# Kernel optimization log

Measured on AMD Instinct MI355X. Metric: run time of the kernel, lower is better.

## Reference

```python
import jax, jax.numpy as jnp
import numpy as np

B = 256          # graphs per batch
NN = 400         # ROI nodes per graph (N*(N-1)/2 = 79800 = input_dim)
HID = [32, 64, 128]
KS = [200, 100, 50]   # nodes kept after each TopKPooling (ratio 0.5 each)
EPS = 1e-5


def setup_inputs() -> dict:
    key = jax.random.key(0)
    ks = jax.random.split(key, 20)
    # flattened strict upper triangle of a nonnegative FC matrix per sample
    data = jax.random.uniform(ks[0], (B, NN * (NN - 1) // 2), dtype=jnp.float32)
    inp = {"data": data}
    dims = [1] + HID
    for l in range(3):
        fan_in = dims[l]
        inp[f"W{l+1}"] = jax.random.normal(ks[1 + 5 * l], (dims[l], dims[l + 1]), jnp.float32) / np.sqrt(fan_in)
        inp[f"b{l+1}"] = jnp.zeros((dims[l + 1],), jnp.float32)
        inp[f"g{l+1}"] = jnp.ones((dims[l + 1],), jnp.float32)      # BN gamma
        inp[f"be{l+1}"] = jnp.zeros((dims[l + 1],), jnp.float32)    # BN beta
        inp[f"p{l+1}"] = jax.random.normal(ks[4 + 5 * l], (dims[l + 1],), jnp.float32) * 0.1  # TopK score vector
    return inp


def _gcn_conv(A, X, W, b):
    # GCNConv with edge weights: add self loops (weight 1), symmetric D^-1/2 A D^-1/2
    n = A.shape[1]
    Al = A + jnp.eye(n, dtype=A.dtype)[None]          # (B, n, n)
    deg = Al.sum(axis=-1)                             # (B, n)
    dis = jnp.where(deg > 0, jax.lax.rsqrt(deg), 0.0)
    An = dis[:, :, None] * Al * dis[:, None, :]
    return jnp.einsum('bij,bjf->bif', An, X @ W) + b


def _block(A, X, W, b, g, be, p, k):
    # GCNConv -> ReLU -> BatchNorm(train stats) -> (dropout=identity) -> TopKPooling
    h = jax.nn.relu(_gcn_conv(A, X, W, b))
    mu = h.mean(axis=(0, 1))
    var = h.var(axis=(0, 1))
    h = (h - mu) * jax.lax.rsqrt(var + EPS) * g + be
    # TopKPooling: score = x . p / ||p||, keep top k per graph, gate by tanh(score)
    score = h @ p / jnp.linalg.norm(p)                # (B, n)
    vals, idx = jax.lax.top_k(score, k)               # (B, k)
    Xn = jnp.take_along_axis(h, idx[:, :, None], axis=1) * jnp.tanh(vals)[:, :, None]
    bi = jnp.arange(A.shape[0])[:, None, None]
    An = A[bi, idx[:, :, None], idx[:, None, :]]      # filter_adj: edges among kept nodes
    return An, Xn


def reference(data, W1, b1, g1, be1, p1, W2, b2, g2, be2, p2, W3, b3, g3, be3, p3):
    Bn = data.shape[0]
    iu0, iu1 = np.triu_indices(NN, 1)
    A = jnp.zeros((Bn, NN, NN), data.dtype).at[:, iu0, iu1].set(data)
    A = A + jnp.swapaxes(A, 1, 2)                     # symmetric FC adjacency, zero diag
    X = jnp.ones((Bn, NN, 1), data.dtype)             # initial node feature dim = 1
    A, X = _block(A, X, W1, b1, g1, be1, p1, KS[0])
    A, X = _block(A, X, W2, b2, g2, be2, p2, KS[1])
    A, X = _block(A, X, W3, b3, g3, be3, p3, KS[2])
    return X.max(axis=1)                              # global_max_pool -> (B, 128)
```

## Files before the change

kernel.cpp:

```cpp
#include <hip/hip_runtime.h>
#include <math.h>

#define BB   256
#define NN0  400
#define NE   79800
#define EPSF 1e-5f

__device__ __forceinline__ int tri_e(int a, int c) {
  return a*(NN0-1) - ((a*(a-1))>>1) + (c - a - 1);
}

__device__ __forceinline__ size_t PRI(int b, int ti, int tj, int r) {
  return (((size_t)b*7 + ti)*7 + tj)*64 + r;
}

__device__ __forceinline__ float wave_sum(float v) {
  #pragma unroll
  for (int o = 32; o > 0; o >>= 1) v += __shfl_xor(v, o, 64);
  return v;
}

__device__ __forceinline__ void bitonic_desc(float* sc, int* si, int P) {
  const int tid = threadIdx.x;
  const int nt = blockDim.x;
  for (int k = 2; k <= P; k <<= 1) {
    for (int j = k >> 1; j > 0; j >>= 1) {
      __syncthreads();
      for (int i = tid; i < P; i += nt) {
        int ixj = i ^ j;
        if (ixj > i) {
          float a = sc[i], c = sc[ixj];
          int ai = si[i], ci = si[ixj];
          bool bef = (a > c) || (a == c && ai < ci);
          bool sw = ((i & k) == 0) ? !bef : bef;
          if (sw) { sc[i] = c; sc[ixj] = a; si[i] = ci; si[ixj] = ai; }
        }
      }
    }
  }
  __syncthreads();
}

__global__ __launch_bounds__(256) void k_tri_mv(
    const float* __restrict__ data,
    const float* __restrict__ pr_in, const float* __restrict__ pc_in,
    float* __restrict__ pr, float* __restrict__ pc) {
  __shared__ float tile[64][65];
  __shared__ float dI[64], dJ[64];
  const int q0 = blockIdx.x % 7, b = blockIdx.x / 7;
  const int tid = threadIdx.x;
  const int wave = tid >> 6, lane = tid & 63;
  const float* __restrict__ drow = data + (size_t)b*NE;
  int ti_a[4], tj_a[4];
  #pragma unroll
  for (int u = 0; u < 4; ++u) {
    int t = q0 + u*7;
    int ti = 0, rem = t;
    while (rem >= 7 - ti) { rem -= 7 - ti; ++ti; }
    ti_a[u] = ti; tj_a[u] = ti + rem;
  }
  float vreg[16];
  float rI = 0.f, rJ = 0.f;
  auto issue = [&](int u) {
    const int i0 = ti_a[u]*64, j0 = tj_a[u]*64;
    const int ni = min(64, NN0 - i0), nj = min(64, NN0 - j0);
    #pragma unroll
    for (int k = 0; k < 16; ++k) {
      const int rr = wave*16 + k;
      const int i = i0 + rr, j = j0 + lane;
      vreg[k] = 0.f;
      if (rr < ni && lane < nj && j > i) vreg[k] = drow[tri_e(i, j)];
    }
    if (pr_in) {
      if (tid < 64) {
        float a = 0.f;
        if (tid < ni) {
          const int tt = ti_a[u], r = tid;
          float acc = 1.f;
          for (int tj = tt; tj < 7; ++tj) acc += pr_in[PRI(b, tt, tj, r)];
          for (int ts = 0; ts <= tt; ++ts) acc += pc_in[PRI(b, ts, tt, r)];
          a = rsqrtf(acc);
        }
        rI = a;
      } else if (tid < 128) {
        const int c = tid - 64;
        float a = 0.f;
        if (c < nj) {
          const int tt = tj_a[u], r = c;
          float acc = 1.f;
          for (int tj = tt; tj < 7; ++tj) acc += pr_in[PRI(b, tt, tj, r)];
          for (int ts = 0; ts <= tt; ++ts) acc += pc_in[PRI(b, ts, tt, r)];
          a = rsqrtf(acc);
        }
        rJ = a;
      }
    } else {
      if (tid < 64) rI = (tid < ni) ? 1.f : 0.f;
      else if (tid < 128) rJ = (tid - 64 < nj) ? 1.f : 0.f;
    }
  };
  issue(0);
  #pragma unroll 1
  for (int u = 0; u < 4; ++u) {
    const int ti = ti_a[u], tj = tj_a[u];
    if (u) __syncthreads();
    #pragma unroll
    for (int k = 0; k < 16; ++k) tile[wave*16 + k][lane] = vreg[k];
    if (tid < 64) dI[tid] = rI;
    else if (tid < 128) dJ[tid-64] = rJ;
    __syncthreads();
    if (u + 1 < 4) issue(u + 1);
    {
      const int r = tid >> 2, q = tid & 3;
      float s = 0.f;
      #pragma unroll
      for (int c = 0; c < 16; ++c) s += tile[r][q*16 + c] * dJ[q*16 + c];
      s += __shfl_xor(s, 1, 64);
      s += __shfl_xor(s, 2, 64);
      if (q == 0) pr[PRI(b, ti, tj, r)] = s;
    }
    {
      const int c = tid >> 2, q = tid & 3;
      float s = 0.f;
      #pragma unroll
      for (int r = 0; r < 16; ++r) s += tile[q*16 + r][c] * dI[q*16 + r];
      s += __shfl_xor(s, 1, 64);
      s += __shfl_xor(s, 2, 64);
      if (q == 0) pc[PRI(b, ti, tj, c)] = s;
    }
  }
}

__global__ __launch_bounds__(256) void k_sfin_stats_red(
    const float* __restrict__ pr, const float* __restrict__ pc,
    const float* __restrict__ pr2, const float* __restrict__ pc2,
    const float* __restrict__ W1, const float* __restrict__ b1,
    float* __restrict__ s1, float* __restrict__ acc1) {
  __shared__ float sl[256];
  __shared__ float st[64];
  __shared__ float w1s[32], b1s[32];
  const int tid = threadIdx.x;
  const int i = blockIdx.x*256 + tid;
  if (tid < 32) { w1s[tid] = W1[tid]; b1s[tid] = b1[tid]; }
  if (tid < 64) st[tid] = 0.f;
  const int b = i / NN0, n = i % NN0;
  const int t = n >> 6, r = n & 63;
  float dacc = 1.f, sacc = 0.f;
  for (int tj = t; tj < 7; ++tj) { dacc += pr[PRI(b, t, tj, r)]; sacc += pr2[PRI(b, t, tj, r)]; }
  for (int ti = 0; ti <= t; ++ti) { dacc += pc[PRI(b, ti, t, r)]; sacc += pc2[PRI(b, ti, t, r)]; }
  const float d = rsqrtf(dacc);
  const float s = d * (d + sacc);
  s1[i] = s;
  sl[tid] = s;
  __syncthreads();
  const int f = tid & 31, sub = tid >> 5;
  const float w = w1s[f], bb = b1s[f];
  float S = 0.f, Q = 0.f;
  #pragma unroll
  for (int k = 0; k < 32; ++k) {
    const float ss = sl[sub*32 + k];
    const float h = fmaxf(ss*w + bb, 0.f);
    S += h; Q += h*h;
  }
  atomicAdd(&st[f], S);
  atomicAdd(&st[32+f], Q);
  __syncthreads();
  if (tid < 64) atomicAdd(&acc1[tid], st[tid]);
}

__global__ __launch_bounds__(512) void k_top1(
    const float* __restrict__ s1, const float* __restrict__ acc1,
    const float* __restrict__ W1, const float* __restrict__ b1,
    const float* __restrict__ g1, const float* __restrict__ be1,
    const float* __restrict__ p1, const float* __restrict__ W2,
    int* __restrict__ nodes2, int* __restrict__ sperm2, float* __restrict__ Y2) {
  __shared__ float sc[512]; __shared__ int si[512];
  __shared__ float sS[NN0];
  __shared__ float tvs[200];
  __shared__ int nds_l[200];
  __shared__ float w1s[32], b1s[32], cfs[32], scs[32], shs[32];
  __shared__ __align__(16) float hp[6400];
  __shared__ float c0s;
  const int tid = threadIdx.x, b = blockIdx.x;
  if (tid < 32) { w1s[tid] = W1[tid]; b1s[tid] = b1[tid]; }
  if (tid < 64) {
    float scale = 0.f, shift = 0.f, pv = 0.f;
    if (tid < 32) {
      const float S = acc1[tid], Q = acc1[32 + tid];
      const float N = 102400.f;
      const float mu = S / N;
      const float var = Q / N - mu*mu;
      const float inv = rsqrtf(var + EPSF);
      scale = inv * g1[tid];
      shift = be1[tid] - mu * scale;
      pv = p1[tid];
    }
    const float pn = sqrtf(wave_sum(pv*pv));
    if (tid < 32) { scs[tid] = scale; shs[tid] = shift; cfs[tid] = scale*pv/pn; }
    float u = (tid < 32) ? shift*pv/pn : 0.f;
    u = wave_sum(u);
    if (tid == 0) c0s = u;
  }
  __syncthreads();
  const float c0 = c0s;
  for (int i = tid; i < 512; i += 512) {
    if (i < NN0) {
      const float s = s1[(size_t)b*NN0 + i];
      sS[i] = s;
      float sco = c0;
      #pragma unroll
      for (int f = 0; f < 32; ++f) sco += fmaxf(s*w1s[f] + b1s[f], 0.f) * cfs[f];
      sc[i] = sco; si[i] = i;
    } else { sc[i] = -INFINITY; si[i] = 0x7fffffff; }
  }
  bitonic_desc(sc, si, 512);
  for (int k = tid; k < 200; k += 512) {
    tvs[k] = tanhf(sc[k]);
    nds_l[k] = si[k];
    nodes2[b*200 + k] = si[k];
  }
  __syncthreads();
  for (int o = tid; o < 6400; o += 512) {
    const int k = o >> 5, f = o & 31;
    const float s = sS[nds_l[k]];
    const float h = fmaxf(s*w1s[f] + b1s[f], 0.f);
    hp[o] = (h*scs[f] + shs[f]) * tvs[k];
  }
  __syncthreads();
  {
    const int g = tid & 63;
    float wr[32];
    #pragma unroll
    for (int f = 0; f < 32; ++f) wr[f] = W2[f*64 + g];
    for (int o = tid; o < 12800; o += 512) {
      const int k = o >> 6;
      float acc = 0.f;
      #pragma unroll
      for (int c4 = 0; c4 < 8; ++c4) {
        const float4 x4 = *(const float4*)&hp[(k<<5) + (c4<<2)];
        acc += x4.x*wr[c4*4] + x4.y*wr[c4*4+1] + x4.z*wr[c4*4+2] + x4.w*wr[c4*4+3];
      }
      Y2[(size_t)b*12800 + o] = acc;
    }
  }
  __syncthreads();
  if (tid < 256) {
    sc[tid] = (tid < 200) ? -(float)nds_l[tid] : -INFINITY;
    si[tid] = (tid < 200) ? tid : 0x7fffffff;
  }
  bitonic_desc(sc, si, 256);
  if (tid < 200) sperm2[b*200 + tid] = si[tid];
}

__global__ __launch_bounds__(256) void k_gatherA2(
    const float* __restrict__ data, const int* __restrict__ nodes2,
    const int* __restrict__ sperm2, float* __restrict__ A2, float* __restrict__ dis2) {
  __shared__ int nds[200], sp[200], sn[200];
  __shared__ float rowbuf[4][200];
  const int idx = blockIdx.x;
  const int r9 = idx >> 3;
  const int b = (idx & 7)*32 + r9/50;
  const int rg = r9 % 50;
  const int tid = threadIdx.x;
  if (tid < 200) { nds[tid] = nodes2[b*200 + tid]; sp[tid] = sperm2[b*200 + tid]; }
  __syncthreads();
  if (tid < 200) sn[tid] = nds[sp[tid]];
  __syncthreads();
  const int wave = tid >> 6, lane = tid & 63;
  const int i = rg*4 + wave;
  const int ni = nds[i];
  const float* __restrict__ drow = data + (size_t)b*NE;
  float accd = 0.f;
  for (int jj = lane; jj < 200; jj += 64) {
    const int sj = sn[jj];
    float v = 0.f;
    if (sj != ni) {
      const int a = min(ni, sj), c = max(ni, sj);
      v = drow[tri_e(a, c)];
    }
    rowbuf[wave][sp[jj]] = v;
    accd += v;
  }
  __syncthreads();
  for (int j = lane; j < 200; j += 64)
    A2[((size_t)b*200 + i)*200 + j] = rowbuf[wave][j];
  accd = wave_sum(accd);
  if (lane == 0) dis2[b*200 + i] = rsqrtf(1.f + accd);
}

__global__ __launch_bounds__(256) void k_conv2(
    const float* __restrict__ A2, const float* __restrict__ Y2,
    const float* __restrict__ dis2, const float* __restrict__ b2,
    float* __restrict__ h2g, float* __restrict__ acc2g) {
  __shared__ __align__(16) float zb[40*64];
  __shared__ __align__(16) float ab[40*32];
  __shared__ float st[128];
  const int tid = threadIdx.x;
  const int b = blockIdx.x / 7, p = blockIdx.x % 7;
  const int wave = tid >> 6, lane = tid & 63;
  const int r0 = p*32;
  if (tid < 128) st[tid] = 0.f;
  const float bl = b2[lane];
  float acc[8] = {0,0,0,0,0,0,0,0};
  #pragma unroll 1
  for (int s = 0; s < 5; ++s) {
    const int j0 = s*40;
    if (s) __syncthreads();
    for (int t = tid; t < 640; t += 256) {
      const int js = t >> 4, f4 = t & 15;
      const float dz = dis2[b*200 + j0 + js];
      float4 v = *(const float4*)&Y2[((size_t)b*200 + (j0 + js))*64 + (f4 << 2)];
      v.x *= dz; v.y *= dz; v.z *= dz; v.w *= dz;
      *(float4*)&zb[(js << 6) + (f4 << 2)] = v;
    }
    for (int t = tid; t < 320; t += 256) {
      const int js = t >> 3, c4 = t & 7;
      const int col = r0 + (c4 << 2);
      float4 v = make_float4(0.f, 0.f, 0.f, 0.f);
      if (col <= 196)
        v = *(const float4*)&A2[((size_t)b*200 + (j0 + js))*200 + col];
      *(float4*)&ab[(js << 5) + (c4 << 2)] = v;
    }
    __syncthreads();
    #pragma unroll 4
    for (int js = 0; js < 40; ++js) {
      const float z = zb[(js << 6) + lane];
      const float4 a0 = *(const float4*)&ab[(js << 5) + (wave << 3)];
      const float4 a1 = *(const float4*)&ab[(js << 5) + (wave << 3) + 4];
      acc[0] += a0.x*z; acc[1] += a0.y*z; acc[2] += a0.z*z; acc[3] += a0.w*z;
      acc[4] += a1.x*z; acc[5] += a1.y*z; acc[6] += a1.z*z; acc[7] += a1.w*z;
    }
  }
  float ss = 0.f, qq = 0.f;
  #pragma unroll
  for (int k = 0; k < 8; ++k) {
    const int r = r0 + (wave << 3) + k;
    if (r < 200) {
      const float d = dis2[b*200 + r];
      const float y = Y2[((size_t)b*200 + r)*64 + lane];
      const float h = fmaxf(d*acc[k] + d*d*y + bl, 0.f);
      h2g[((size_t)b*200 + r)*64 + lane] = h;
      ss += h; qq += h*h;
    }
  }
  atomicAdd(&st[lane], ss);
  atomicAdd(&st[64 + lane], qq);
  __syncthreads();
  if (tid < 128) atomicAdd(&acc2g[tid], st[tid]);
}

__global__ __launch_bounds__(512) void k_top2(
    const float* __restrict__ h2g, const float* __restrict__ acc2,
    const float* __restrict__ g2, const float* __restrict__ be2,
    const float* __restrict__ p2, const float* __restrict__ W3,
    const int* __restrict__ nodes2, int* __restrict__ nodes3,
    float* __restrict__ Y3) {
  __shared__ float sc[256]; __shared__ int si[256];
  __shared__ __align__(16) float xs[6400];
  __shared__ float sc2[64], sh2[64], cf2[64];
  __shared__ float c20s;
  const int tid = threadIdx.x, b = blockIdx.x;
  if (tid < 64) {
    const float S = acc2[tid], Q = acc2[64 + tid];
    const float N = 51200.f;
    const float mu = S/N, var = Q/N - mu*mu, inv = rsqrtf(var + EPSF);
    const float scale = inv*g2[tid], shift = be2[tid] - mu*scale;
    const float pv = p2[tid];
    const float pn = sqrtf(wave_sum(pv*pv));
    sc2[tid] = scale; sh2[tid] = shift; cf2[tid] = scale*pv/pn;
    const float u = wave_sum(shift*pv/pn);
    if (tid == 0) c20s = u;
  }
  __syncthreads();
  const int wave = tid >> 6, lane = tid & 63;
  const float cf = cf2[lane];
  const float c20 = c20s;
  for (int i = wave; i < 200; i += 8) {
    float v = h2g[((size_t)b*200 + i)*64 + lane] * cf;
    v = wave_sum(v);
    if (lane == 0) { sc[i] = v + c20; si[i] = i; }
  }
  if (tid >= 200 && tid < 256) { sc[tid] = -INFINITY; si[tid] = 0x7fffffff; }
  bitonic_desc(sc, si, 256);
  const float scale = sc2[lane], shift = sh2[lane];
  for (int o = tid; o < 6400; o += 512) {
    const int k = o >> 6;
    const int idx = si[k];
    const float tv = tanhf(sc[k]);
    xs[o] = (h2g[((size_t)b*200 + idx)*64 + lane] * scale + shift) * tv;
  }
  for (int k = tid; k < 100; k += 512) nodes3[b*100 + k] = nodes2[b*200 + si[k]];
  __syncthreads();
  {
    const int g = tid & 127;
    float wr[64];
    #pragma unroll
    for (int f = 0; f < 64; ++f) wr[f] = W3[f*128 + g];
    for (int o = tid; o < 12800; o += 512) {
      const int k = o >> 7;
      float acc = 0.f;
      #pragma unroll
      for (int c4 = 0; c4 < 16; ++c4) {
        const float4 x4 = *(const float4*)&xs[(k<<6) + (c4<<2)];
        acc += x4.x*wr[c4*4] + x4.y*wr[c4*4+1] + x4.z*wr[c4*4+2] + x4.w*wr[c4*4+3];
      }
      Y3[(size_t)b*12800 + o] = acc;
    }
  }
}

__global__ __launch_bounds__(256) void k_gatherA3(
    const float* __restrict__ data, const int* __restrict__ nodes3,
    float* __restrict__ A3, float* __restrict__ dis3) {
  __shared__ int nds[100];
  const int b = blockIdx.x / 25, rg = blockIdx.x % 25;
  const int tid = threadIdx.x;
  if (tid < 100) nds[tid] = nodes3[b*100 + tid];
  __syncthreads();
  const int wave = tid >> 6, lane = tid & 63;
  const int i = rg*4 + wave;
  const int ni = nds[i];
  const float* __restrict__ drow = data + (size_t)b*NE;
  float accd = 0.f;
  for (int j = lane; j < 100; j += 64) {
    float v = 0.f;
    if (j != i) {
      const int nj = nds[j];
      const int a = min(ni, nj), c = max(ni, nj);
      v = drow[tri_e(a, c)];
    }
    A3[((size_t)b*100 + i)*100 + j] = v;
    accd += v;
  }
  accd = wave_sum(accd);
  if (lane == 0) dis3[b*100 + i] = rsqrtf(1.f + accd);
}

__global__ __launch_bounds__(256) void k_conv3(
    const float* __restrict__ A3, const float* __restrict__ Y3,
    const float* __restrict__ dis3, const float* __restrict__ b3,
    float* __restrict__ h3g, float* __restrict__ acc3g) {
  __shared__ __align__(16) float zb[25*128];
  __shared__ __align__(16) float ab[25*16];
  __shared__ float st[256];
  const int tid = threadIdx.x;
  const int b = blockIdx.x / 7, p = blockIdx.x % 7;
  const int wave = tid >> 6, lane = tid & 63;
  const int r0 = p*16;
  st[tid] = 0.f;
  const float bl0 = b3[lane], bl1 = b3[64 + lane];
  float acc0[4] = {0,0,0,0}, acc1[4] = {0,0,0,0};
  #pragma unroll 1
  for (int s = 0; s < 4; ++s) {
    const int j0 = s*25;
    if (s) __syncthreads();
    for (int t = tid; t < 800; t += 256) {
      const int js = t >> 5, f4 = t & 31;
      const float dz = dis3[b*100 + j0 + js];
      float4 v = *(const float4*)&Y3[((size_t)b*100 + (j0 + js))*128 + (f4 << 2)];
      v.x *= dz; v.y *= dz; v.z *= dz; v.w *= dz;
      *(float4*)&zb[(js << 7) + (f4 << 2)] = v;
    }
    for (int t = tid; t < 100; t += 256) {
      const int js = t >> 2, c4 = t & 3;
      const int col = r0 + (c4 << 2);
      float4 v = make_float4(0.f, 0.f, 0.f, 0.f);
      if (col <= 96)
        v = *(const float4*)&A3[((size_t)b*100 + (j0 + js))*100 + col];
      *(float4*)&ab[(js << 4) + (c4 << 2)] = v;
    }
    __syncthreads();
    #pragma unroll 5
    for (int js = 0; js < 25; ++js) {
      const float z0 = zb[(js << 7) + lane];
      const float z1 = zb[(js << 7) + 64 + lane];
      const float4 a4 = *(const float4*)&ab[(js << 4) + (wave << 2)];
      acc0[0] += a4.x*z0; acc0[1] += a4.y*z0; acc0[2] += a4.z*z0; acc0[3] += a4.w*z0;
      acc1[0] += a4.x*z1; acc1[1] += a4.y*z1; acc1[2] += a4.z*z1; acc1[3] += a4.w*z1;
    }
  }
  float ss0 = 0.f, qq0 = 0.f, ss1 = 0.f, qq1 = 0.f;
  #pragma unroll
  for (int k = 0; k < 4; ++k) {
    const int r = r0 + (wave << 2) + k;
    if (r < 100) {
      const float d = dis3[b*100 + r];
      const float y0 = Y3[((size_t)b*100 + r)*128 + lane];
      const float y1 = Y3[((size_t)b*100 + r)*128 + 64 + lane];
      const float h0 = fmaxf(d*acc0[k] + d*d*y0 + bl0, 0.f);
      const float h1 = fmaxf(d*acc1[k] + d*d*y1 + bl1, 0.f);
      h3g[((size_t)b*100 + r)*128 + lane] = h0;
      h3g[((size_t)b*100 + r)*128 + 64 + lane] = h1;
      ss0 += h0; qq0 += h0*h0; ss1 += h1; qq1 += h1*h1;
    }
  }
  atomicAdd(&st[lane], ss0);
  atomicAdd(&st[64 + lane], ss1);
  atomicAdd(&st[128 + lane], qq0);
  atomicAdd(&st[192 + lane], qq1);
  __syncthreads();
  atomicAdd(&acc3g[tid], st[tid]);
}

__global__ __launch_bounds__(256) void k_top3(
    const float* __restrict__ h3g, const float* __restrict__ acc3,
    const float* __restrict__ g3, const float* __restrict__ be3,
    const float* __restrict__ p3, float* __restrict__ out) {
  __shared__ float sc[128]; __shared__ int si[128]; __shared__ float tv[64];
  __shared__ float scl[128], shl[128], cfl[128];
  __shared__ float red2[4];
  const int tid = threadIdx.x, b = blockIdx.x;
  const int wave = tid >> 6, lane = tid & 63;
  float scale = 0.f, shift = 0.f, pv = 0.f;
  if (tid < 128) {
    const float S = acc3[tid], Q = acc3[128 + tid];
    const float N = 25600.f;
    const float mu = S/N, var = Q/N - mu*mu, inv = rsqrtf(var + EPSF);
    scale = inv*g3[tid]; shift = be3[tid] - mu*scale; pv = p3[tid];
    const float t2 = wave_sum(pv*pv);
    if (lane == 0) red2[wave] = t2;
  }
  __syncthreads();
  const float pn = sqrtf(red2[0] + red2[1]);
  if (tid < 128) {
    scl[tid] = scale; shl[tid] = shift; cfl[tid] = scale*pv/pn;
    const float u = wave_sum(shift*pv/pn);
    if (lane == 0) red2[2 + wave] = u;
  }
  __syncthreads();
  const float c30 = red2[2] + red2[3];
  const float clo = cfl[lane], chi = cfl[64 + lane];
  for (int i = wave; i < 100; i += 4) {
    const float* hr = h3g + ((size_t)b*100 + i)*128;
    float v = hr[lane]*clo + hr[64 + lane]*chi;
    v = wave_sum(v);
    if (lane == 0) { sc[i] = v + c30; si[i] = i; }
  }
  if (tid >= 100 && tid < 128) { sc[tid] = -INFINITY; si[tid] = 0x7fffffff; }
  bitonic_desc(sc, si, 128);
  if (tid < 50) tv[tid] = tanhf(sc[tid]);
  __syncthreads();
  if (tid < 128) {
    const float scalev = scl[tid], shiftv = shl[tid];
    float m = -INFINITY;
    for (int k = 0; k < 50; ++k) {
      const float h = h3g[((size_t)b*100 + si[k])*128 + tid];
      m = fmaxf(m, (h*scalev + shiftv)*tv[k]);
    }
    out[(size_t)b*128 + tid] = m;
  }
}

extern "C" void kernel_launch(void* const* d_in, const int* in_sizes, int n_in,
                              void* d_out, int out_size, void* d_ws, size_t ws_size,
                              hipStream_t stream) {
  (void)in_sizes; (void)n_in; (void)out_size; (void)ws_size;
  const float* data = (const float*)d_in[0];
  const float* W1 = (const float*)d_in[1];
  const float* b1 = (const float*)d_in[2];
  const float* g1 = (const float*)d_in[3];
  const float* be1 = (const float*)d_in[4];
  const float* p1 = (const float*)d_in[5];
  const float* W2 = (const float*)d_in[6];
  const float* b2 = (const float*)d_in[7];
  const float* g2 = (const float*)d_in[8];
  const float* be2 = (const float*)d_in[9];
  const float* p2 = (const float*)d_in[10];
  const float* W3 = (const float*)d_in[11];
  const float* b3 = (const float*)d_in[12];
  const float* g3 = (const float*)d_in[13];
  const float* be3 = (const float*)d_in[14];
  const float* p3 = (const float*)d_in[15];
  float* out = (float*)d_out;

  char* ws = (char*)d_ws;
  size_t off = 0;
  auto alloc = [&](size_t n) { size_t o = off; off += (n + 255) & ~(size_t)255; return o; };
  float* pr     = (float*)(ws + alloc((size_t)BB*49*64*4));
  float* pc     = (float*)(ws + alloc((size_t)BB*49*64*4));
  float* pr2    = (float*)(ws + alloc((size_t)BB*49*64*4));
  float* pc2    = (float*)(ws + alloc((size_t)BB*49*64*4));
  float* s1     = (float*)(ws + alloc((size_t)BB*NN0*4));
  float* accz   = (float*)(ws + alloc(448*4));
  int*   nodes2 = (int*)  (ws + alloc((size_t)BB*200*4));
  int*   sperm2 = (int*)  (ws + alloc((size_t)BB*200*4));
  float* Y2     = (float*)(ws + alloc((size_t)BB*12800*4));
  float* A2     = (float*)(ws + alloc((size_t)BB*40000*4));
  float* dis2   = (float*)(ws + alloc((size_t)BB*200*4));
  float* h2     = (float*)(ws + alloc((size_t)BB*12800*4));
  int*   nodes3 = (int*)  (ws + alloc((size_t)BB*100*4));
  float* Y3     = (float*)(ws + alloc((size_t)BB*12800*4));
  float* A3     = (float*)(ws + alloc((size_t)BB*10000*4));
  float* dis3   = (float*)(ws + alloc((size_t)BB*100*4));
  float* h3     = (float*)(ws + alloc((size_t)BB*12800*4));
  float* acc1 = accz;
  float* acc2 = accz + 64;
  float* acc3 = accz + 192;

  hipMemsetAsync(accz, 0, 448*4, stream);
  k_tri_mv<<<dim3(BB*7), dim3(256), 0, stream>>>(data, nullptr, nullptr, pr, pc);
  k_tri_mv<<<dim3(BB*7), dim3(256), 0, stream>>>(data, pr, pc, pr2, pc2);
  k_sfin_stats_red<<<dim3(400), dim3(256), 0, stream>>>(pr, pc, pr2, pc2, W1, b1, s1, acc1);
  k_top1<<<dim3(BB), dim3(512), 0, stream>>>(s1, acc1, W1, b1, g1, be1, p1, W2, nodes2, sperm2, Y2);
  k_gatherA2<<<dim3(BB*50), dim3(256), 0, stream>>>(data, nodes2, sperm2, A2, dis2);
  k_conv2<<<dim3(BB*7), dim3(256), 0, stream>>>(A2, Y2, dis2, b2, h2, acc2);
  k_top2<<<dim3(BB), dim3(512), 0, stream>>>(h2, acc2, g2, be2, p2, W3, nodes2, nodes3, Y3);
  k_gatherA3<<<dim3(BB*25), dim3(256), 0, stream>>>(data, nodes3, A3, dis3);
  k_conv3<<<dim3(BB*7), dim3(256), 0, stream>>>(A3, Y3, dis3, b3, h3, acc3);
  k_top3<<<dim3(BB), dim3(256), 0, stream>>>(h3, acc3, g3, be3, p3, out);
}
```

Baseline: 482.8 us.

## Restructure GCN conv kernels with full-graph LDS staging and XCD-aware block mapping

The layer-2 and layer-3 convolution kernels now stage the whole dis-scaled feature matrix of a graph in LDS and use two blocks per graph instead of seven. Each wave loads one adjacency row slice per step into lanes and broadcasts the values with readlane into 25 or 13 register accumulators, with a one-step prefetch of the next row. This removes the repeated per-chunk staging and barriers. Several kernels also remap blockIdx so that all blocks of a graph land on the same XCD, which should improve L2 locality. The trade-off is fewer blocks, heavier register use and large LDS footprints, which may lower occupancy.

```diff
diff --git a/kernel.cpp b/kernel.cpp
--- a/kernel.cpp
+++ b/kernel.cpp
@@ -18,6 +18,10 @@
   #pragma unroll
   for (int o = 32; o > 0; o >>= 1) v += __shfl_xor(v, o, 64);
   return v;
+}
+
+__device__ __forceinline__ float rdlane(float v, int k) {
+  return __int_as_float(__builtin_amdgcn_readlane(__float_as_int(v), k));
 }
 
 __device__ __forceinline__ void bitonic_desc(float* sc, int* si, int P) {
@@ -47,7 +51,8 @@
     float* __restrict__ pr, float* __restrict__ pc) {
   __shared__ float tile[64][65];
   __shared__ float dI[64], dJ[64];
-  const int q0 = blockIdx.x % 7, b = blockIdx.x / 7;
+  const int xcd = blockIdx.x & 7, slot = blockIdx.x >> 3;
+  const int b = xcd*32 + slot/7, q0 = slot % 7;
   const int tid = threadIdx.x;
   const int wave = tid >> 6, lane = tid & 63;
   const float* __restrict__ drow = data + (size_t)b*NE;
@@ -181,7 +186,8 @@
   __shared__ float w1s[32], b1s[32], cfs[32], scs[32], shs[32];
   __shared__ __align__(16) float hp[6400];
   __shared__ float c0s;
-  const int tid = threadIdx.x, b = blockIdx.x;
+  const int tid = threadIdx.x;
+  const int b = (blockIdx.x & 7)*32 + (blockIdx.x >> 3);
   if (tid < 32) { w1s[tid] = W1[tid]; b1s[tid] = b1[tid]; }
   if (tid < 64) {
     float scale = 0.f, shift = 0.f, pv = 0.f;
@@ -203,7 +209,8 @@
   }
   __syncthreads();
   const float c0 = c0s;
-  for (int i = tid; i < 512; i += 512) {
+  {
+    const int i = tid;
     if (i < NN0) {
       const float s = s1[(size_t)b*NN0 + i];
       sS[i] = s;
@@ -292,56 +299,49 @@
     const float* __restrict__ A2, const float* __restrict__ Y2,
     const float* __restrict__ dis2, const float* __restrict__ b2,
     float* __restrict__ h2g, float* __restrict__ acc2g) {
-  __shared__ __align__(16) float zb[40*64];
-  __shared__ __align__(16) float ab[40*32];
+  __shared__ __align__(16) float zb[200*64];
+  __shared__ float dsb[200];
   __shared__ float st[128];
   const int tid = threadIdx.x;
-  const int b = blockIdx.x / 7, p = blockIdx.x % 7;
+  const int xcd = blockIdx.x & 7, slot = blockIdx.x >> 3;
+  const int b = xcd*32 + (slot >> 1), p = slot & 1;
   const int wave = tid >> 6, lane = tid & 63;
-  const int r0 = p*32;
   if (tid < 128) st[tid] = 0.f;
+  if (tid < 200) dsb[tid] = dis2[b*200 + tid];
+  for (int t = tid; t < 3200; t += 256) {
+    const int row = t >> 4, f4 = t & 15;
+    const float dz = dis2[b*200 + row];
+    float4 v = *(const float4*)&Y2[((size_t)b*200 + row)*64 + (f4 << 2)];
+    v.x *= dz; v.y *= dz; v.z *= dz; v.w *= dz;
+    *(float4*)&zb[(row << 6) + (f4 << 2)] = v;
+  }
   const float bl = b2[lane];
-  float acc[8] = {0,0,0,0,0,0,0,0};
-  #pragma unroll 1
-  for (int s = 0; s < 5; ++s) {
-    const int j0 = s*40;
-    if (s) __syncthreads();
-    for (int t = tid; t < 640; t += 256) {
-      const int js = t >> 4, f4 = t & 15;
-      const float dz = dis2[b*200 + j0 + js];
-      float4 v = *(const float4*)&Y2[((size_t)b*200 + (j0 + js))*64 + (f4 << 2)];
-      v.x *= dz; v.y *= dz; v.z *= dz; v.w *= dz;
-      *(float4*)&zb[(js << 6) + (f4 << 2)] = v;
-    }
-    for (int t = tid; t < 320; t += 256) {
-      const int js = t >> 3, c4 = t & 7;
-      const int col = r0 + (c4 << 2);
-      float4 v = make_float4(0.f, 0.f, 0.f, 0.f);
-      if (col <= 196)
-        v = *(const float4*)&A2[((size_t)b*200 + (j0 + js))*200 + col];
-      *(float4*)&ab[(js << 5) + (c4 << 2)] = v;
-    }
-    __syncthreads();
-    #pragma unroll 4
-    for (int js = 0; js < 40; ++js) {
-      const float z = zb[(js << 6) + lane];
-      const float4 a0 = *(const float4*)&ab[(js << 5) + (wave << 3)];
-      const float4 a1 = *(const float4*)&ab[(js << 5) + (wave << 3) + 4];
-      acc[0] += a0.x*z; acc[1] += a0.y*z; acc[2] += a0.z*z; acc[3] += a0.w*z;
-      acc[4] += a1.x*z; acc[5] += a1.y*z; acc[6] += a1.z*z; acc[7] += a1.w*z;
-    }
+  __syncthreads();
+  const int rb = p*100 + wave*25;
+  auto ldA = [&](int j) -> float {
+    return (lane < 25) ? A2[((size_t)b*200 + j)*200 + rb + lane] : 0.f;
+  };
+  float acc[25];
+  #pragma unroll
+  for (int k = 0; k < 25; ++k) acc[k] = 0.f;
+  float a_cur = ldA(0);
+  #pragma unroll 2
+  for (int j = 0; j < 200; ++j) {
+    const float a_nxt = (j < 199) ? ldA(j + 1) : 0.f;
+    const float z = zb[(j << 6) + lane];
+    #pragma unroll
+    for (int k = 0; k < 25; ++k)
+      acc[k] = fmaf(rdlane(a_cur, k), z, acc[k]);
+    a_cur = a_nxt;
   }
   float ss = 0.f, qq = 0.f;
   #pragma unroll
-  for (int k = 0; k < 8; ++k) {
-    const int r = r0 + (wave << 3) + k;
-    if (r < 200) {
-      const float d = dis2[b*200 + r];
-      const float y = Y2[((size_t)b*200 + r)*64 + lane];
-      const float h = fmaxf(d*acc[k] + d*d*y + bl, 0.f);
-      h2g[((size_t)b*200 + r)*64 + lane] = h;
-      ss += h; qq += h*h;
-    }
+  for (int k = 0; k < 25; ++k) {
+    const int r = rb + k;
+    const float d = dsb[r];
+    const float h = fmaxf(d*(acc[k] + zb[(r << 6) + lane]) + bl, 0.f);
+    h2g[((size_t)b*200 + r)*64 + lane] = h;
+    ss += h; qq += h*h;
   }
   atomicAdd(&st[lane], ss);
   atomicAdd(&st[64 + lane], qq);
@@ -359,7 +359,8 @@
   __shared__ __align__(16) float xs[6400];
   __shared__ float sc2[64], sh2[64], cf2[64];
   __shared__ float c20s;
-  const int tid = threadIdx.x, b = blockIdx.x;
+  const int tid = threadIdx.x;
+  const int b = (blockIdx.x & 7)*32 + (blockIdx.x >> 3);
   if (tid < 64) {
     const float S = acc2[tid], Q = acc2[64 + tid];
     const float N = 51200.f;
@@ -413,7 +414,8 @@
     const float* __restrict__ data, const int* __restrict__ nodes3,
     float* __restrict__ A3, float* __restrict__ dis3) {
   __shared__ int nds[100];
-  const int b = blockIdx.x / 25, rg = blockIdx.x % 25;
+  const int slot = blockIdx.x >> 3;
+  const int b = (blockIdx.x & 7)*32 + slot/25, rg = slot % 25;
   const int tid = threadIdx.x;
   if (tid < 100) nds[tid] = nodes3[b*100 + tid];
   __syncthreads();
@@ -440,55 +442,56 @@
     const float* __restrict__ A3, const float* __restrict__ Y3,
     const float* __restrict__ dis3, const float* __restrict__ b3,
     float* __restrict__ h3g, float* __restrict__ acc3g) {
-  __shared__ __align__(16) float zb[25*128];
-  __shared__ __align__(16) float ab[25*16];
+  __shared__ __align__(16) float zb[100*128];
+  __shared__ float dsb[100];
   __shared__ float st[256];
   const int tid = threadIdx.x;
-  const int b = blockIdx.x / 7, p = blockIdx.x % 7;
+  const int xcd = blockIdx.x & 7, slot = blockIdx.x >> 3;
+  const int b = xcd*32 + (slot >> 1), p = slot & 1;
   const int wave = tid >> 6, lane = tid & 63;
-  const int r0 = p*16;
   st[tid] = 0.f;
+  if (tid < 100) dsb[tid] = dis3[b*100 + tid];
+  for (int t = tid; t < 3200; t += 256) {
+    const int row = t >> 5, f4 = t & 31;
+    const float dz = dis3[b*100 + row];
+    float4 v = *(const float4*)&Y3[((size_t)b*100 + row)*128 + (f4 << 2)];
+    v.x *= dz; v.y *= dz; v.z *= dz; v.w *= dz;
+    *(float4*)&zb[(row << 7) + (f4 << 2)] = v;
+  }
   const float bl0 = b3[lane], bl1 = b3[64 + lane];
-  float acc0[4] = {0,0,0,0}, acc1[4] = {0,0,0,0};
-  #pragma unroll 1
-  for (int s = 0; s < 4; ++s) {
-    const int j0 = s*25;
-    if (s) __syncthreads();
-    for (int t = tid; t < 800; t += 256) {
-      const int js = t >> 5, f4 = t & 31;
-      const float dz = dis3[b*100 + j0 + js];
-      float4 v = *(const float4*)&Y3[((size_t)b*100 + (j0 + js))*128 + (f4 << 2)];
-      v.x *= dz; v.y *= dz; v.z *= dz; v.w *= dz;
-      *(float4*)&zb[(js << 7) + (f4 << 2)] = v;
-    }
-    for (int t = tid; t < 100; t += 256) {
-      const int js = t >> 2, c4 = t & 3;
-      const int col = r0 + (c4 << 2);
-      float4 v = make_float4(0.f, 0.f, 0.f, 0.f);
-      if (col <= 96)
-        v = *(const float4*)&A3[((size_t)b*100 + (j0 + js))*100 + col];
-      *(float4*)&ab[(js << 4) + (c4 << 2)] = v;
-    }
-    __syncthreads();
-    #pragma unroll 5
-    for (int js = 0; js < 25; ++js) {
-      const float z0 = zb[(js << 7) + lane];
-      const float z1 = zb[(js << 7) + 64 + lane];
-      const float4 a4 = *(const float4*)&ab[(js << 4) + (wave << 2)];
-      acc0[0] += a4.x*z0; acc0[1] += a4.y*z0; acc0[2] += a4.z*z0; acc0[3] += a4.w*z0;
-      acc1[0] += a4.x*z1; acc1[1] += a4.y*z1; acc1[2] += a4.z*z1; acc1[3] += a4.w*z1;
-    }
+  __syncthreads();
+  const int rb = p*50;
+  const int lw = wave*13;
+  auto ldA = [&](int j) -> float {
+    return (lane < 13 && lw + lane < 50)
+      ? A3[((size_t)b*100 + j)*100 + rb + lw + lane] : 0.f;
+  };
+  float acc0[13], acc1[13];
+  #pragma unroll
+  for (int k = 0; k < 13; ++k) { acc0[k] = 0.f; acc1[k] = 0.f; }
+  float a_cur = ldA(0);
+  #pragma unroll 2
+  for (int j = 0; j < 100; ++j) {
+    const float a_nxt = (j < 99) ? ldA(j + 1) : 0.f;
+    const float z0 = zb[(j << 7) + lane];
+    const float z1 = zb[(j << 7) + 64 + lane];
+    #pragma unroll
+    for (int k = 0; k < 13; ++k) {
+      const float av = rdlane(a_cur, k);
+      acc0[k] = fmaf(av, z0, acc0[k]);
+      acc1[k] = fmaf(av, z1, acc1[k]);
+    }
+    a_cur = a_nxt;
   }
   float ss0 = 0.f, qq0 = 0.f, ss1 = 0.f, qq1 = 0.f;
   #pragma unroll
-  for (int k = 0; k < 4; ++k) {
-    const int r = r0 + (wave << 2) + k;
-    if (r < 100) {
-      const float d = dis3[b*100 + r];
-      const float y0 = Y3[((size_t)b*100 + r)*128 + lane];
-      const float y1 = Y3[((size_t)b*100 + r)*128 + 64 + lane];
-      const float h0 = fmaxf(d*acc0[k] + d*d*y0 + bl0, 0.f);
-      const float h1 = fmaxf(d*acc1[k] + d*d*y1 + bl1, 0.f);
+  for (int k = 0; k < 13; ++k) {
+    const int lr = lw + k;
+    if (lr < 50) {
+      const int r = rb + lr;
+      const float d = dsb[r];
+      const float h0 = fmaxf(d*(acc0[k] + zb[(r << 7) + lane]) + bl0, 0.f);
+      const float h1 = fmaxf(d*(acc1[k] + zb[(r << 7) + 64 + lane]) + bl1, 0.f);
       h3g[((size_t)b*100 + r)*128 + lane] = h0;
       h3g[((size_t)b*100 + r)*128 + 64 + lane] = h1;
       ss0 += h0; qq0 += h0*h0; ss1 += h1; qq1 += h1*h1;
@@ -509,7 +512,8 @@
   __shared__ float sc[128]; __shared__ int si[128]; __shared__ float tv[64];
   __shared__ float scl[128], shl[128], cfl[128];
   __shared__ float red2[4];
-  const int tid = threadIdx.x, b = blockIdx.x;
+  const int tid = threadIdx.x;
+  const int b = (blockIdx.x & 7)*32 + (blockIdx.x >> 3);
   const int wave = tid >> 6, lane = tid & 63;
   float scale = 0.f, shift = 0.f, pv = 0.f;
   if (tid < 128) {
@@ -603,9 +607,9 @@
   k_sfin_stats_red<<<dim3(400), dim3(256), 0, stream>>>(pr, pc, pr2, pc2, W1, b1, s1, acc1);
   k_top1<<<dim3(BB), dim3(512), 0, stream>>>(s1, acc1, W1, b1, g1, be1, p1, W2, nodes2, sperm2, Y2);
   k_gatherA2<<<dim3(BB*50), dim3(256), 0, stream>>>(data, nodes2, sperm2, A2, dis2);
-  k_conv2<<<dim3(BB*7), dim3(256), 0, stream>>>(A2, Y2, dis2, b2, h2, acc2);
+  k_conv2<<<dim3(BB*2), dim3(256), 0, stream>>>(A2, Y2, dis2, b2, h2, acc2);
   k_top2<<<dim3(BB), dim3(512), 0, stream>>>(h2, acc2, g2, be2, p2, W3, nodes2, nodes3, Y3);
   k_gatherA3<<<dim3(BB*25), dim3(256), 0, stream>>>(data, nodes3, A3, dis3);
-  k_conv3<<<dim3(BB*7), dim3(256), 0, stream>>>(A3, Y3, dis3, b3, h3, acc3);
+  k_conv3<<<dim3(BB*2), dim3(256), 0, stream>>>(A3, Y3, dis3, b3, h3, acc3);
   k_top3<<<dim3(BB), dim3(256), 0, stream>>>(h3, acc3, g3, be3, p3, out);
 }
```

Measured after the change: 433.1 us. 1.11x faster.
